# Kernel optimization log

Measured on AMD Instinct MI355X. Metric: run time of the kernel, lower is better.

The kernel has to match this reference:

```python
import jax, jax.numpy as jnp
import numpy as np

# NTU-25 joint groupings (0-indexed)
BODY_GROUP = [np.array([5,6,7,8,22,23])-1, np.array([9,10,11,12,24,25])-1,
              np.array([13,14,15,16])-1, np.array([17,18,19,20])-1,
              np.array([1,2,3,4,21])-1]
PART_GROUP = [np.array([1,2,21])-1, np.array([3,4])-1, np.array([5,6,7])-1,
              np.array([8,22,23])-1, np.array([9,10,11])-1, np.array([12,24,25])-1,
              np.array([13,14])-1, np.array([15,16])-1, np.array([17,18])-1,
              np.array([19,20])-1]

def _corr_joints(parts):
    num_joints = max(max(p) for p in parts) + 1
    res = []
    for i in range(num_joints):
        for j, p in enumerate(parts):
            if i in p:
                res.append(j)
                break
    return np.asarray(res, dtype=np.int32)

JOINTS_PART = _corr_joints(PART_GROUP)  # [25] -> part id in [0,10)
JOINTS_BODY = _corr_joints(BODY_GROUP)  # [25] -> body id in [0,5)

N, C, T, V, S = 64, 96, 128, 25, 3

def setup_inputs() -> dict:
    key = jax.random.key(0)
    ks = jax.random.split(key, 10)
    x = jax.random.normal(ks[0], (N, C, T, V), jnp.float32)
    p_att = jax.random.normal(ks[1], (N, S, 10, 10), jnp.float32)
    b_att = jax.random.normal(ks[2], (N, S, 5, 5), jnp.float32)
    w_in = jax.random.normal(ks[3], (3 * C, C), jnp.float32) * (1.0 / np.sqrt(C))
    b_in = jax.random.normal(ks[4], (3 * C,), jnp.float32) * 0.01
    w_ff = jax.random.normal(ks[5], (C, C), jnp.float32) * (1.0 / np.sqrt(C))
    b_ff = jax.random.normal(ks[6], (C,), jnp.float32) * 0.01
    bn_gamma = jnp.ones((C,), jnp.float32)
    bn_beta = jnp.zeros((C,), jnp.float32)
    bn_mean = jnp.zeros((C,), jnp.float32)
    bn_var = jnp.ones((C,), jnp.float32)
    return {"x": x, "p_att": p_att, "b_att": b_att, "w_in": w_in, "b_in": b_in,
            "w_ff": w_ff, "b_ff": b_ff, "bn_gamma": bn_gamma, "bn_beta": bn_beta,
            "bn_mean": bn_mean, "bn_var": bn_var}

def reference(x, p_att, b_att, w_in, b_in, w_ff, b_ff, bn_gamma, bn_beta, bn_mean, bn_var):
    n, c, t, v = x.shape
    s = S
    mid = c // s
    jp = jnp.asarray(JOINTS_PART)
    jb = jnp.asarray(JOINTS_BODY)
    # 1x1 conv -> QKV: [N, 3C, T, V] viewed as [N, 3, S, mid, T, V]
    qkv = jnp.einsum('nctv,oc->notv', x, w_in) + b_in[None, :, None, None]
    qkv = qkv.reshape(n, 3, s, mid, t, v)
    q, k, val = qkv[:, 0], qkv[:, 1], qkv[:, 2]
    att = jnp.tanh(jnp.einsum('nsctu,nsctv->nsuv', q, k) / (mid * t))
    # structured gather of part/body biases to joint-level [N,S,V,V]
    pp = p_att[:, :, jp[:, None], jp[None, :]]
    bb = b_att[:, :, jb[:, None], jb[None, :]]
    att = att + pp + bb
    y = jnp.einsum('nsuv,nsctv->nsctu', att, val).reshape(n, c, t, v)
    # ff_nets: 1x1 conv + BatchNorm (eval mode, running stats)
    y = jnp.einsum('nctv,oc->notv', y, w_ff) + b_ff[None, :, None, None]
    inv = bn_gamma / jnp.sqrt(bn_var + 1e-5)
    y = (y - bn_mean[None, :, None, None]) * inv[None, :, None, None] + bn_beta[None, :, None, None]
    return jax.nn.leaky_relu(x + y, 0.1)
```

## Files before the change

kernel.cpp:

```cpp
#include <hip/hip_runtime.h>
#include <cmath>

#define NN 64
#define CC 96
#define TT 128
#define VV 25
#define SS 3
#define TB 4
#define NTB (TT/TB)
#define ROWS (TB*VV)

#define XFP 104
#define X3P 104
#define QKP 200
#define YP  104
#define WLP 104

typedef __attribute__((ext_vector_type(8))) __bf16 bf16x8;
typedef __attribute__((ext_vector_type(4))) float f32x4;

#define MFMA16(a,b,c) __builtin_amdgcn_mfma_f32_16x16x32_bf16((a),(b),(c),0,0,0)

__constant__ int JP[25] = {0,0,1,1,2,2,2,3,4,4,4,5,6,6,7,7,8,8,9,9,0,3,3,5,5};
__constant__ int JB[25] = {4,4,4,4,0,0,0,0,1,1,1,1,2,2,2,2,3,3,3,3,4,0,0,1,1};

__device__ inline unsigned short f2b(float f) {
  unsigned int u = __float_as_uint(f);
  u += 0x7fffu + ((u >> 16) & 1u);
  return (unsigned short)(u >> 16);
}
__device__ inline bf16x8 ldbf8(const unsigned short* p) {
  union { uint4 u; bf16x8 b; } z;
  z.u = *(const uint4*)p;
  return z.b;
}
__device__ inline f32x4 fz() {
  f32x4 z; z[0] = 0.f; z[1] = 0.f; z[2] = 0.f; z[3] = 0.f; return z;
}

__global__ __launch_bounds__(256) void k0(
    const float* __restrict__ w_in, const float* __restrict__ w_ff,
    const float* __restrict__ b_ff, const float* __restrict__ gam,
    const float* __restrict__ bet, const float* __restrict__ mea,
    const float* __restrict__ var,
    unsigned short* __restrict__ wbin, unsigned short* __restrict__ wbff,
    float* __restrict__ scsh)
{
  int i = blockIdx.x * 256 + threadIdx.x;
  if (i < 288 * 96) wbin[i] = f2b(w_in[i]);
  if (i < 96 * 96)  wbff[i] = f2b(w_ff[i]);
  if (i < 96) {
    float sc = gam[i] * rsqrtf(var[i] + 1e-5f);
    scsh[i]      = sc;
    scsh[96 + i] = (b_ff[i] - mea[i]) * sc + bet[i];
  }
}

__global__ __launch_bounds__(256, 2) void k1(
    const float* __restrict__ x, const unsigned short* __restrict__ wbin,
    const float* __restrict__ b_in, float* __restrict__ partG,
    unsigned short* __restrict__ val_ws)
{
  __shared__ __align__(16) unsigned short xT32[128 * X3P];
  __shared__ __align__(16) unsigned short qk[128 * QKP];
  __shared__ float bL[192];
  unsigned short* xf   = qk;
  unsigned short* valL = qk;

  const int tid  = threadIdx.x;
  const int wid  = tid >> 6, lane = tid & 63;
  const int lrow = lane & 15;
  const int lk8  = (lane >> 4) << 3;
  const int ldr4 = (lane >> 4) << 2;
  const int tb = blockIdx.x & (NTB - 1);
  const int n  = blockIdx.x >> 5;
  const int t0 = tb * TB;

  const float* xb = x + (size_t)n * CC * TT * VV + (size_t)t0 * VV;
  for (int e = tid; e < CC * (ROWS / 4); e += 256) {
    int i4 = e % (ROWS / 4), c = e / (ROWS / 4);
    float4 v = *(const float4*)&xb[(size_t)c * (TT * VV) + i4 * 4];
    ushort4 h;
    h.x = f2b(v.x); h.y = f2b(v.y); h.z = f2b(v.z); h.w = f2b(v.w);
    *(ushort4*)&xf[c * XFP + i4 * 4] = h;
  }
  for (int e = tid; e < 28 * 13; e += 256) {
    int pr = e / 13, q = e % 13;
    int row = (pr / 7) * 32 + 25 + (pr % 7);
    uint4 z; z.x = 0u; z.y = 0u; z.z = 0u; z.w = 0u;
    *(uint4*)&xT32[row * X3P + q * 8] = z;
  }
  if (tid < 192) bL[tid] = b_in[tid];
  __syncthreads();

  for (int e = tid; e < ROWS * (CC / 4); e += 256) {
    int i = e % ROWS, c4 = e / ROWS;
    int row = (i / VV) * 32 + (i % VV);
    ushort4 h;
    h.x = xf[(c4 * 4 + 0) * XFP + i];
    h.y = xf[(c4 * 4 + 1) * XFP + i];
    h.z = xf[(c4 * 4 + 2) * XFP + i];
    h.w = xf[(c4 * 4 + 3) * XFP + i];
    *(ushort4*)&xT32[row * X3P + c4 * 4] = h;
  }
  __syncthreads();

  f32x4 acc[3][8];
  #pragma unroll
  for (int i = 0; i < 3; ++i)
    #pragma unroll
    for (int nf = 0; nf < 8; ++nf) acc[i][nf] = fz();

  #pragma unroll
  for (int ks = 0; ks < 3; ++ks) {
    bf16x8 a[3];
    #pragma unroll
    for (int i = 0; i < 3; ++i)
      a[i] = ldbf8(&wbin[((wid * 3 + i) * 16 + lrow) * 96 + ks * 32 + lk8]);
    #pragma unroll
    for (int nf = 0; nf < 8; ++nf) {
      bf16x8 b = ldbf8(&xT32[(nf * 16 + lrow) * X3P + ks * 32 + lk8]);
      #pragma unroll
      for (int i = 0; i < 3; ++i)
        acc[i][nf] = MFMA16(a[i], b, acc[i][nf]);
    }
  }
  #pragma unroll
  for (int i = 0; i < 3; ++i) {
    int ob = (wid * 3 + i) * 16 + ldr4;
    float4 bb = *(const float4*)&bL[ob];
    #pragma unroll
    for (int nf = 0; nf < 8; ++nf) {
      int col = nf * 16 + lrow;
      ushort4 h;
      h.x = f2b(acc[i][nf][0] + bb.x);
      h.y = f2b(acc[i][nf][1] + bb.y);
      h.z = f2b(acc[i][nf][2] + bb.z);
      h.w = f2b(acc[i][nf][3] + bb.w);
      *(ushort4*)&qk[col * QKP + ob] = h;
    }
  }
  __syncthreads();

  f32x4 vacc[2][6];
  #pragma unroll
  for (int m = 0; m < 2; ++m)
    #pragma unroll
    for (int of = 0; of < 6; ++of) vacc[m][of] = fz();
  #pragma unroll
  for (int ks = 0; ks < 3; ++ks) {
    bf16x8 bw[6];
    #pragma unroll
    for (int of = 0; of < 6; ++of)
      bw[of] = ldbf8(&wbin[(192 + of * 16 + lrow) * 96 + ks * 32 + lk8]);
    #pragma unroll
    for (int m = 0; m < 2; ++m) {
      bf16x8 a = ldbf8(&xT32[((wid + m * 4) * 16 + lrow) * X3P + ks * 32 + lk8]);
      #pragma unroll
      for (int of = 0; of < 6; ++of)
        vacc[m][of] = MFMA16(a, bw[of], vacc[m][of]);
    }
  }

  if (wid < 3) {
    const int s = wid;
    f32x4 g[2][2];
    g[0][0] = fz(); g[0][1] = fz(); g[1][0] = fz(); g[1][1] = fz();
    #pragma unroll
    for (int dt = 0; dt < TB; ++dt) {
      int r0 = dt * 32;
      bf16x8 a0 = ldbf8(&qk[(r0 + lrow) * QKP + s * 32 + lk8]);
      bf16x8 a1 = ldbf8(&qk[(r0 + 16 + lrow) * QKP + s * 32 + lk8]);
      bf16x8 b0 = ldbf8(&qk[(r0 + lrow) * QKP + 96 + s * 32 + lk8]);
      bf16x8 b1 = ldbf8(&qk[(r0 + 16 + lrow) * QKP + 96 + s * 32 + lk8]);
      g[0][0] = MFMA16(a0, b0, g[0][0]);
      g[0][1] = MFMA16(a0, b1, g[0][1]);
      g[1][0] = MFMA16(a1, b0, g[1][0]);
      g[1][1] = MFMA16(a1, b1, g[1][1]);
    }
    float* pg = partG + ((size_t)tb * (NN * SS) + (n * SS + s)) * (VV * VV);
    #pragma unroll
    for (int mi = 0; mi < 2; ++mi)
      #pragma unroll
      for (int ni = 0; ni < 2; ++ni)
        #pragma unroll
        for (int r = 0; r < 4; ++r) {
          int u = mi * 16 + ldr4 + r, v = ni * 16 + lrow;
          if (u < VV && v < VV) pg[u * VV + v] = g[mi][ni][r];
        }
  }
  __syncthreads();

  float bv[6];
  #pragma unroll
  for (int of = 0; of < 6; ++of) bv[of] = b_in[192 + of * 16 + lrow];
  #pragma unroll
  for (int m = 0; m < 2; ++m) {
    int i0 = (wid + m * 4) * 16 + ldr4;
    #pragma unroll
    for (int of = 0; of < 6; ++of) {
      int cout = of * 16 + lrow;
      ushort4 h;
      h.x = f2b(vacc[m][of][0] + bv[of]);
      h.y = f2b(vacc[m][of][1] + bv[of]);
      h.z = f2b(vacc[m][of][2] + bv[of]);
      h.w = f2b(vacc[m][of][3] + bv[of]);
      *(ushort4*)&valL[cout * 128 + i0] = h;
    }
  }
  __syncthreads();

  for (int e = tid; e < 1536; e += 256) {
    int c4 = e & 3, t = (e >> 2) & 3, cout = e >> 4;
    uint4 w = *(uint4*)&valL[cout * 128 + t * 32 + c4 * 8];
    if (c4 == 3) { w.x &= 0xFFFFu; w.y = 0u; w.z = 0u; w.w = 0u; }
    *(uint4*)&val_ws[(((size_t)(n * 96 + cout)) * TT + (t0 + t)) * 32 + c4 * 8] = w;
  }
}

__global__ __launch_bounds__(256) void k2(
    const float* __restrict__ partG, const float* __restrict__ p_att,
    const float* __restrict__ b_att, unsigned short* __restrict__ att)
{
  const int ns = blockIdx.x;
  for (int e = threadIdx.x; e < 1024; e += 256) {
    int u = e >> 5, v = e & 31;
    float a = 0.f;
    if (u < VV && v < VV) {
      float g = 0.f;
      #pragma unroll 4
      for (int tb = 0; tb < NTB; ++tb)
        g += partG[((size_t)tb * (NN * SS) + ns) * (VV * VV) + u * VV + v];
      a = tanhf(g * (1.0f / 4096.0f))
        + p_att[(size_t)ns * 100 + JP[u] * 10 + JP[v]]
        + b_att[(size_t)ns * 25  + JB[u] * 5  + JB[v]];
    }
    att[(size_t)ns * 1024 + e] = f2b(a);
  }
}

__global__ __launch_bounds__(256, 3) void k3(
    const float* __restrict__ x, const unsigned short* __restrict__ val_ws,
    const unsigned short* __restrict__ wbff, const float* __restrict__ scsh,
    const unsigned short* __restrict__ att, float* __restrict__ out)
{
  __shared__ __align__(16) unsigned short yL[112 * YP];
  __shared__ __align__(16) unsigned short wL[96 * WLP];

  const int tid  = threadIdx.x;
  const int wid  = tid >> 6, lane = tid & 63;
  const int lrow = lane & 15;
  const int lk8  = (lane >> 4) << 3;
  const int ldr4 = (lane >> 4) << 2;
  const int tb = blockIdx.x & (NTB - 1);
  const int n  = blockIdx.x >> 5;
  const int t0 = tb * TB;
  const int t  = t0 + wid;

  for (int e = tid; e < 96 * 12; e += 256) {
    int r = e / 12, q = e % 12;
    *(uint4*)&wL[r * WLP + q * 8] = *(const uint4*)&wbff[(size_t)r * 96 + q * 8];
  }

  const unsigned short* attn = att + (size_t)n * SS * 1024;
  f32x4 pacc[3][2][2];
  #pragma unroll
  for (int s = 0; s < 3; ++s)
    #pragma unroll
    for (int mi = 0; mi < 2; ++mi)
      #pragma unroll
      for (int uf = 0; uf < 2; ++uf) pacc[s][mi][uf] = fz();

  #pragma unroll
  for (int s = 0; s < 3; ++s) {
    bf16x8 av[2], bu[2];
    #pragma unroll
    for (int mi = 0; mi < 2; ++mi) {
      int c = s * 32 + mi * 16 + lrow;
      av[mi] = ldbf8(&val_ws[(((size_t)(n * 96 + c)) * TT + t) * 32 + lk8]);
    }
    #pragma unroll
    for (int uf = 0; uf < 2; ++uf)
      bu[uf] = ldbf8(&attn[s * 1024 + (uf * 16 + lrow) * 32 + lk8]);
    #pragma unroll
    for (int mi = 0; mi < 2; ++mi)
      #pragma unroll
      for (int uf = 0; uf < 2; ++uf)
        pacc[s][mi][uf] = MFMA16(av[mi], bu[uf], pacc[s][mi][uf]);
  }

  #pragma unroll
  for (int s = 0; s < 3; ++s)
    #pragma unroll
    for (int mi = 0; mi < 2; ++mi)
      #pragma unroll
      for (int uf = 0; uf < 2; ++uf) {
        int u = uf * 16 + lrow;
        if (u < VV) {
          int c0 = s * 32 + mi * 16 + ldr4;
          ushort4 h;
          h.x = f2b(pacc[s][mi][uf][0]);
          h.y = f2b(pacc[s][mi][uf][1]);
          h.z = f2b(pacc[s][mi][uf][2]);
          h.w = f2b(pacc[s][mi][uf][3]);
          *(ushort4*)&yL[(wid * VV + u) * YP + c0] = h;
        }
      }
  __syncthreads();

  #pragma unroll
  for (int rep = 0; rep < 2; ++rep) {
    int nf = wid + rep * 4;
    if (nf < 7) {
      f32x4 facc[6];
      #pragma unroll
      for (int of = 0; of < 6; ++of) facc[of] = fz();
      #pragma unroll
      for (int ks = 0; ks < 3; ++ks) {
        bf16x8 by = ldbf8(&yL[(nf * 16 + lrow) * YP + ks * 32 + lk8]);
        #pragma unroll
        for (int of = 0; of < 6; ++of) {
          bf16x8 aw = ldbf8(&wL[(of * 16 + lrow) * WLP + ks * 32 + lk8]);
          facc[of] = MFMA16(aw, by, facc[of]);
        }
      }
      int i = nf * 16 + lrow;
      if (i < ROWS) {
        size_t base = (size_t)n * CC * (TT * VV) + (size_t)t0 * VV + i;
        #pragma unroll
        for (int of = 0; of < 6; ++of) {
          int o0 = of * 16 + ldr4;
          float4 sc = *(const float4*)&scsh[o0];
          float4 sh = *(const float4*)&scsh[96 + o0];
          const float* scp = (const float*)&sc;
          const float* shp = (const float*)&sh;
          #pragma unroll
          for (int r = 0; r < 4; ++r) {
            size_t idx = base + (size_t)(o0 + r) * (TT * VV);
            float z = facc[of][r] * scp[r] + shp[r] + x[idx];
            out[idx] = (z >= 0.f) ? z : 0.1f * z;
          }
        }
      }
    }
  }
}

extern "C" void kernel_launch(void* const* d_in, const int* in_sizes, int n_in,
                              void* d_out, int out_size, void* d_ws, size_t ws_size,
                              hipStream_t stream)
{
  const float* x     = (const float*)d_in[0];
  const float* p_att = (const float*)d_in[1];
  const float* b_att = (const float*)d_in[2];
  const float* w_in  = (const float*)d_in[3];
  const float* b_in  = (const float*)d_in[4];
  const float* w_ff  = (const float*)d_in[5];
  const float* b_ff  = (const float*)d_in[6];
  const float* gam   = (const float*)d_in[7];
  const float* bet   = (const float*)d_in[8];
  const float* mea   = (const float*)d_in[9];
  const float* var   = (const float*)d_in[10];
  float* out = (float*)d_out;

  char* ws = (char*)d_ws;
  unsigned short* wbin = (unsigned short*)ws;
  unsigned short* wbff = wbin + 288 * 96;
  unsigned short* attw = wbff + 96 * 96;
  float* scsh  = (float*)(ws + 466944);
  float* partG = (float*)(ws + 467712);
  unsigned short* val_ws = (unsigned short*)(ws + 15827712);

  k0<<<108, 256, 0, stream>>>(w_in, w_ff, b_ff, gam, bet, mea, var,
                              wbin, wbff, scsh);
  k1<<<NN * NTB, 256, 0, stream>>>(x, wbin, b_in, partG, val_ws);
  k2<<<NN * SS, 256, 0, stream>>>(partG, p_att, b_att, attw);
  k3<<<NN * NTB, 256, 0, stream>>>(x, val_ws, wbff, scsh, attw, out);
}
```

Before: 130.9 us.

## Store V in MFMA fragment order to skip LDS transpose and barriers

k1 now writes the bias-added V projection to global memory straight from the MFMA accumulator registers, in a fragment-native tiled layout. This removes the LDS staging buffer, its transpose, the padding mask and two __syncthreads. k3 is changed to read this layout by assembling each bf16x8 operand from two 8-byte loads. The cost is less contiguous 8-byte global accesses, and padded V entries now hold bias values instead of zeros; this relies on the padded attention entries being zero.

```diff
diff --git a/kernel.cpp b/kernel.cpp
--- a/kernel.cpp
+++ b/kernel.cpp
@@ -64,8 +64,7 @@
   __shared__ __align__(16) unsigned short xT32[128 * X3P];
   __shared__ __align__(16) unsigned short qk[128 * QKP];
   __shared__ float bL[192];
-  unsigned short* xf   = qk;
-  unsigned short* valL = qk;
+  unsigned short* xf = qk;
 
   const int tid  = threadIdx.x;
   const int wid  = tid >> 6, lane = tid & 63;
@@ -159,6 +158,25 @@
       #pragma unroll
       for (int of = 0; of < 6; ++of)
         vacc[m][of] = MFMA16(a, bw[of], vacc[m][of]);
+    }
+  }
+  {
+    float bv[6];
+    #pragma unroll
+    for (int of = 0; of < 6; ++of) bv[of] = bL[0] * 0.f + b_in[192 + of * 16 + lrow];
+    unsigned short* vdst = val_ws + (size_t)(n * NTB + tb) * 12288;
+    #pragma unroll
+    for (int m = 0; m < 2; ++m) {
+      int F = wid + m * 4;
+      #pragma unroll
+      for (int of = 0; of < 6; ++of) {
+        ushort4 h;
+        h.x = f2b(vacc[m][of][0] + bv[of]);
+        h.y = f2b(vacc[m][of][1] + bv[of]);
+        h.z = f2b(vacc[m][of][2] + bv[of]);
+        h.w = f2b(vacc[m][of][3] + bv[of]);
+        *(ushort4*)&vdst[((of * 8 + F) * 64 + lane) * 4] = h;
+      }
     }
   }
 
@@ -188,33 +206,6 @@
           int u = mi * 16 + ldr4 + r, v = ni * 16 + lrow;
           if (u < VV && v < VV) pg[u * VV + v] = g[mi][ni][r];
         }
-  }
-  __syncthreads();
-
-  float bv[6];
-  #pragma unroll
-  for (int of = 0; of < 6; ++of) bv[of] = b_in[192 + of * 16 + lrow];
-  #pragma unroll
-  for (int m = 0; m < 2; ++m) {
-    int i0 = (wid + m * 4) * 16 + ldr4;
-    #pragma unroll
-    for (int of = 0; of < 6; ++of) {
-      int cout = of * 16 + lrow;
-      ushort4 h;
-      h.x = f2b(vacc[m][of][0] + bv[of]);
-      h.y = f2b(vacc[m][of][1] + bv[of]);
-      h.z = f2b(vacc[m][of][2] + bv[of]);
-      h.w = f2b(vacc[m][of][3] + bv[of]);
-      *(ushort4*)&valL[cout * 128 + i0] = h;
-    }
-  }
-  __syncthreads();
-
-  for (int e = tid; e < 1536; e += 256) {
-    int c4 = e & 3, t = (e >> 2) & 3, cout = e >> 4;
-    uint4 w = *(uint4*)&valL[cout * 128 + t * 32 + c4 * 8];
-    if (c4 == 3) { w.x &= 0xFFFFu; w.y = 0u; w.z = 0u; w.w = 0u; }
-    *(uint4*)&val_ws[(((size_t)(n * 96 + cout)) * TT + (t0 + t)) * 32 + c4 * 8] = w;
   }
 }
 
@@ -250,12 +241,12 @@
   const int tid  = threadIdx.x;
   const int wid  = tid >> 6, lane = tid & 63;
   const int lrow = lane & 15;
-  const int lk8  = (lane >> 4) << 3;
-  const int ldr4 = (lane >> 4) << 2;
+  const int hi   = lane >> 4;
+  const int lk8  = hi << 3;
+  const int ldr4 = hi << 2;
   const int tb = blockIdx.x & (NTB - 1);
   const int n  = blockIdx.x >> 5;
   const int t0 = tb * TB;
-  const int t  = t0 + wid;
 
   for (int e = tid; e < 96 * 12; e += 256) {
     int r = e / 12, q = e % 12;
@@ -263,6 +254,10 @@
   }
 
   const unsigned short* attn = att + (size_t)n * SS * 1024;
+  const unsigned short* vsrc = val_ws + (size_t)(n * NTB + tb) * 12288;
+  const int F = wid * 2 + (hi >> 1);
+  const int cb = ((hi & 1) * 2) * 16 + lrow;
+
   f32x4 pacc[3][2][2];
   #pragma unroll
   for (int s = 0; s < 3; ++s)
@@ -276,8 +271,13 @@
     bf16x8 av[2], bu[2];
     #pragma unroll
     for (int mi = 0; mi < 2; ++mi) {
-      int c = s * 32 + mi * 16 + lrow;
-      av[mi] = ldbf8(&val_ws[(((size_t)(n * 96 + c)) * TT + t) * 32 + lk8]);
+      int of = s * 2 + mi;
+      const unsigned short* p = &vsrc[((of * 8 + F) * 64 + cb) * 4];
+      union { uint4 u; bf16x8 b; } z;
+      uint2 c0 = *(const uint2*)p;
+      uint2 c1 = *(const uint2*)(p + 64);
+      z.u.x = c0.x; z.u.y = c0.y; z.u.z = c1.x; z.u.w = c1.y;
+      av[mi] = z.b;
     }
     #pragma unroll
     for (int uf = 0; uf < 2; ++uf)
```

Result: faster. 120.6 us (-7.8%).
